# Optimization experiments

Measured on AMD Instinct MI355X. Metric: run time of the kernel, lower is better.

## Reference

```python
import jax, jax.numpy as jnp
import numpy as np

DIM = 1024
NH = 16
HD = DIM // NH  # 64
B, S = 4, 2048
EPS = 1e-5


def layer_norm(x, g, b):
    mu = jnp.mean(x, axis=-1, keepdims=True)
    var = jnp.mean(jnp.square(x - mu), axis=-1, keepdims=True)
    return (x - mu) * jax.lax.rsqrt(var + EPS) * g + b


def setup_inputs() -> dict:
    key = jax.random.key(0)
    ks = jax.random.split(key, 12)
    std = 0.02
    return {
        "x": jax.random.normal(ks[0], (B, S, DIM), jnp.float32),
        "ln1_g": jnp.ones((DIM,), jnp.float32),
        "ln1_b": jnp.zeros((DIM,), jnp.float32),
        # per-head Q/K/V linears stacked over heads: [NH, DIM, HD]
        "Wq": jax.random.normal(ks[1], (NH, DIM, HD), jnp.float32) * std,
        "bq": jnp.zeros((NH, HD), jnp.float32),
        "Wk": jax.random.normal(ks[2], (NH, DIM, HD), jnp.float32) * std,
        "bk": jnp.zeros((NH, HD), jnp.float32),
        "Wv": jax.random.normal(ks[3], (NH, DIM, HD), jnp.float32) * std,
        "bv": jnp.zeros((NH, HD), jnp.float32),
        "ln2_g": jnp.ones((DIM,), jnp.float32),
        "ln2_b": jnp.zeros((DIM,), jnp.float32),
        # FC block: LayerNorm -> Linear(dim,4dim) -> GELU -> Linear(4dim,dim) -> GELU
        "fcln_g": jnp.ones((DIM,), jnp.float32),
        "fcln_b": jnp.zeros((DIM,), jnp.float32),
        "W1": jax.random.normal(ks[4], (DIM, 4 * DIM), jnp.float32) * std,
        "b1": jnp.zeros((4 * DIM,), jnp.float32),
        "W2": jax.random.normal(ks[5], (4 * DIM, DIM), jnp.float32) * std,
        "b2": jnp.zeros((DIM,), jnp.float32),
    }


def reference(x, ln1_g, ln1_b, Wq, bq, Wk, bk, Wv, bv,
              ln2_g, ln2_b, fcln_g, fcln_b, W1, b1, W2, b2):
    # --- MHA branch: x + concat_h(head_h(ln1(x))) ---
    h = layer_norm(x, ln1_g, ln1_b)                       # [B,S,D]
    q = jnp.einsum('bsd,hdk->bhsk', h, Wq) + bq[None, :, None, :]
    k = jnp.einsum('bsd,hdk->bhsk', h, Wk) + bk[None, :, None, :]
    v = jnp.einsum('bsd,hdk->bhsk', h, Wv) + bv[None, :, None, :]
    scores = jnp.einsum('bhsk,bhtk->bhst', q, k) / jnp.sqrt(jnp.float32(HD))
    causal = jnp.tril(jnp.ones((S, S), bool))
    scores = jnp.where(causal[None, None], scores, jnp.float32(-1e9))
    attn = jax.nn.softmax(scores, axis=-1)                # [B,NH,S,S]
    o = jnp.einsum('bhst,bhtk->bhsk', attn, v)            # [B,NH,S,HD]
    o = o.transpose(0, 2, 1, 3).reshape(B, S, DIM)        # concat heads
    x = x + o
    # --- FC branch: x + GELU(GELU(LN(ln2(x)) @ W1) @ W2) ---
    h2 = layer_norm(x, ln2_g, ln2_b)
    h2 = layer_norm(h2, fcln_g, fcln_b)
    h2 = jax.nn.gelu(h2 @ W1 + b1, approximate=False)
    h2 = jax.nn.gelu(h2 @ W2 + b2, approximate=False)
    return x + h2
```

## Files before the change

kernel.cpp:

```cpp
#include <hip/hip_runtime.h>
#include <math.h>

#define DIMD 1024
#define NHD  16
#define HDD  64
#define BBB  4
#define SSS  2048
#define MMM  (BBB*SSS)

typedef __bf16 bf16;
typedef __bf16 bf16x8 __attribute__((ext_vector_type(8)));
typedef __bf16 bf16x4 __attribute__((ext_vector_type(4)));
typedef float  f32x4  __attribute__((ext_vector_type(4)));


__device__ __forceinline__ void gld16(const void* g, void* l) {
  __builtin_amdgcn_global_load_lds((const __attribute__((address_space(1))) void*)g,
                                   (__attribute__((address_space(3))) void*)l,
                                   16, 0, 0);
}

__device__ __forceinline__ f32x4 mfma_bf16(bf16x8 a, bf16x8 b, f32x4 c) {
  return __builtin_amdgcn_mfma_f32_16x16x32_bf16(a, b, c, 0, 0, 0);
}

__device__ __forceinline__ float gelu_f(float x) {
  const float u2 = 1.5957691216057308f * x * (1.0f + 0.044715f * x * x);
  const float e = __expf(u2);
  float r;
  asm("v_rcp_f32 %0, %1" : "=v"(r) : "v"(e + 1.0f));
  return x * (1.0f - r);
}

__device__ __forceinline__ void blockReduce2(float& s, float& s2, float* red) {
  #pragma unroll
  for (int m = 1; m < 64; m <<= 1) {
    s  += __shfl_xor(s,  m);
    s2 += __shfl_xor(s2, m);
  }
  const int wave = threadIdx.x >> 6, lane = threadIdx.x & 63;
  __syncthreads();
  if (lane == 0) { red[wave*2] = s; red[wave*2+1] = s2; }
  __syncthreads();
  s  = red[0] + red[2] + red[4] + red[6];
  s2 = red[1] + red[3] + red[5] + red[7];
}

#define SBAR() do { __builtin_amdgcn_sched_barrier(0); __builtin_amdgcn_s_barrier(); \
                    __builtin_amdgcn_sched_barrier(0); } while (0)
#define LGKM0() do { asm volatile("s_waitcnt lgkmcnt(0)" ::: "memory"); \
                     __builtin_amdgcn_sched_barrier(0); } while (0)
#define VMC(n)  do { asm volatile("s_waitcnt vmcnt(" #n ")" ::: "memory"); \
                     __builtin_amdgcn_sched_barrier(0); } while (0)


__global__ __launch_bounds__(256)
void transpose_k(const float* __restrict__ in, bf16* __restrict__ out, int R, int C) {
  __shared__ float tile[32][33];
  const int z = blockIdx.z;
  in  += (size_t)z * R * C;
  out += (size_t)z * R * C;
  const int r0 = blockIdx.x * 32, c0 = blockIdx.y * 32;
  const int tx = threadIdx.x, ty = threadIdx.y;
  #pragma unroll
  for (int k = 0; k < 4; ++k)
    tile[ty + k*8][tx] = in[(size_t)(r0 + ty + k*8) * C + c0 + tx];
  __syncthreads();
  #pragma unroll
  for (int k = 0; k < 4; ++k)
    out[(size_t)(c0 + ty + k*8) * R + r0 + tx] = (bf16)tile[tx][ty + k*8];
}


__global__ __launch_bounds__(256)
void transpose_qkv_k(const float* __restrict__ Wq, const float* __restrict__ Wk,
                     const float* __restrict__ Wv, bf16* __restrict__ out) {
  __shared__ float tile[32][33];
  const int z = blockIdx.z;
  const int which = z >> 4, zh = z & 15;
  const float* in = (which == 0 ? Wq : (which == 1 ? Wk : Wv)) + (size_t)zh * 1024 * 64;
  bf16* op = out + (size_t)z * 64 * 1024;
  const int r0 = blockIdx.x * 32, c0 = blockIdx.y * 32;
  const int tx = threadIdx.x, ty = threadIdx.y;
  #pragma unroll
  for (int k = 0; k < 4; ++k)
    tile[ty + k*8][tx] = in[(size_t)(r0 + ty + k*8) * 64 + c0 + tx];
  __syncthreads();
  #pragma unroll
  for (int k = 0; k < 4; ++k)
    op[(size_t)(c0 + ty + k*8) * 1024 + r0 + tx] = (bf16)tile[tx][ty + k*8];
}


__global__ __launch_bounds__(256)
void transpose_v_k(const bf16* __restrict__ in, bf16* __restrict__ out) {
  __shared__ bf16 t[64*72];
  const int z = blockIdx.y;
  const int s0 = blockIdx.x * 64;
  const bf16* ip = in + (size_t)z * SSS * HDD + (size_t)s0 * HDD;
  bf16* op = out + (size_t)z * SSS * HDD + s0;
  const int tid = threadIdx.x;
  #pragma unroll
  for (int p = 0; p < 2; ++p) {
    const int r = p*32 + (tid >> 3);
    const int c = (tid & 7) * 8;
    const int cs = c ^ (((r >> 3) & 7) << 3);
    *(bf16x8*)&t[r*72 + cs] = *(const bf16x8*)&ip[(size_t)r * HDD + c];
  }
  __syncthreads();
  #pragma unroll
  for (int p = 0; p < 2; ++p) {
    const int hd = p*32 + (tid >> 3);
    const int c0 = (tid & 7) * 8;
    bf16x8 v;
    #pragma unroll
    for (int j = 0; j < 8; ++j) {
      const int r = c0 + j;
      v[j] = t[r*72 + (hd ^ (((r >> 3) & 7) << 3))];
    }
    *(bf16x8*)&op[(size_t)hd * SSS + c0] = v;
  }
}


__global__ __launch_bounds__(256)
void ln1_k(const float* __restrict__ x, const float* __restrict__ g,
           const float* __restrict__ b, bf16* __restrict__ out) {
  __shared__ float red[8];
  const int row = blockIdx.x, t = threadIdx.x;
  const float4 v = ((const float4*)(x + (size_t)row * DIMD))[t];
  float s  = v.x + v.y + v.z + v.w;
  float s2 = v.x*v.x + v.y*v.y + v.z*v.z + v.w*v.w;
  blockReduce2(s, s2, red);
  const float mu   = s * (1.0f / DIMD);
  const float var  = s2 * (1.0f / DIMD) - mu * mu;
  const float rstd = rsqrtf(var + 1e-5f);
  const float4 gv = ((const float4*)g)[t];
  const float4 bv = ((const float4*)b)[t];
  bf16x4 o;
  o[0] = (bf16)((v.x - mu) * rstd * gv.x + bv.x);
  o[1] = (bf16)((v.y - mu) * rstd * gv.y + bv.y);
  o[2] = (bf16)((v.z - mu) * rstd * gv.z + bv.z);
  o[3] = (bf16)((v.w - mu) * rstd * gv.w + bv.w);
  *(bf16x4*)(out + (size_t)row * DIMD + t*4) = o;
}


__global__ __launch_bounds__(256)
void ln2fc_k(const float* __restrict__ x1,
             const float* __restrict__ g2, const float* __restrict__ b2,
             const float* __restrict__ g3, const float* __restrict__ b3,
             bf16* __restrict__ out) {
  __shared__ float red[8];
  const int row = blockIdx.x, t = threadIdx.x;
  const float4 v = ((const float4*)(x1 + (size_t)row * DIMD))[t];
  float s  = v.x + v.y + v.z + v.w;
  float s2 = v.x*v.x + v.y*v.y + v.z*v.z + v.w*v.w;
  blockReduce2(s, s2, red);
  float mu   = s * (1.0f / DIMD);
  float rstd = rsqrtf(s2 * (1.0f / DIMD) - mu * mu + 1e-5f);
  const float4 gv2 = ((const float4*)g2)[t];
  const float4 bv2 = ((const float4*)b2)[t];
  float y0 = (v.x - mu) * rstd * gv2.x + bv2.x;
  float y1 = (v.y - mu) * rstd * gv2.y + bv2.y;
  float y2 = (v.z - mu) * rstd * gv2.z + bv2.z;
  float y3 = (v.w - mu) * rstd * gv2.w + bv2.w;
  s  = y0 + y1 + y2 + y3;
  s2 = y0*y0 + y1*y1 + y2*y2 + y3*y3;
  blockReduce2(s, s2, red);
  mu   = s * (1.0f / DIMD);
  rstd = rsqrtf(s2 * (1.0f / DIMD) - mu * mu + 1e-5f);
  const float4 gv3 = ((const float4*)g3)[t];
  const float4 bv3 = ((const float4*)b3)[t];
  bf16x4 o;
  o[0] = (bf16)((y0 - mu) * rstd * gv3.x + bv3.x);
  o[1] = (bf16)((y1 - mu) * rstd * gv3.y + bv3.y);
  o[2] = (bf16)((y2 - mu) * rstd * gv3.z + bv3.z);
  o[3] = (bf16)((y3 - mu) * rstd * gv3.w + bv3.w);
  *(bf16x4*)(out + (size_t)row * DIMD + t*4) = o;
}


template<int MH2>
__device__ __forceinline__ void load_aH(bf16x8 (&d)[MH2][2], const bf16* base, int roff,
                                        int qv, int sw) {
  #pragma unroll
  for (int mi = 0; mi < MH2; ++mi)
    #pragma unroll
    for (int kk = 0; kk < 2; ++kk)
      d[mi][kk] = *(const bf16x8*)&base[roff + mi*1024 + (((kk<<2)+qv)^sw)*8];
}

__device__ __forceinline__ void load_b2(bf16x8 (&d)[2][2], const bf16* base, int roff,
                                        int qv, int sw) {
  #pragma unroll
  for (int nj = 0; nj < 2; ++nj)
    #pragma unroll
    for (int kk = 0; kk < 2; ++kk)
      d[nj][kk] = *(const bf16x8*)&base[roff + nj*1024 + (((kk<<2)+qv)^sw)*8];
}

template<int EPI, int MH2>
__global__ __launch_bounds__(512)
void gemm8p(const bf16* __restrict__ A, const bf16* __restrict__ Bt,
            int K, int N, int nbx,
            const float* __restrict__ bias, bf16* __restrict__ outB,
            float* __restrict__ outF,
            const float* __restrict__ bq, const float* __restrict__ bk,
            const float* __restrict__ bv) {
  constexpr int BM = 64 * MH2;
  __shared__ bf16 sA[2][BM*64];
  __shared__ bf16 sB[2][256*64];
  const int tid = threadIdx.x, wave = tid >> 6, lane = tid & 63;
  const int wm = wave >> 2, wn = wave & 3;

  const int q8 = gridDim.x >> 3;
  const int wg = (blockIdx.x & 7) * q8 + (blockIdx.x >> 3);
  const int by = wg / nbx, bx = wg - by * nbx;
  const int row0 = by * BM, col0 = bx * 256;

  const int l8 = lane >> 3, l7 = lane & 7;
  const int gsw = (l7 ^ l8) * 8;
  const int lo = lane & 15, qv = lane >> 4, sw = lane & 7;

  const bf16* Ags = A  + (size_t)(row0 + wave*8 + l8) * K + gsw;
  const bf16* Bgs = Bt + (size_t)(col0 + wave*8 + l8) * K + gsw;

  #define STAGE_A(buf, r, kt) gld16(Ags + (size_t)(r)*64*K + (kt), &sA[buf][(r)*4096 + wave*512])
  #define STAGE_B(buf, r, kt) gld16(Bgs + (size_t)(r)*64*K + (kt), &sB[buf][(r)*4096 + wave*512])

  const int fA = (wm*(32*MH2) + lo) * 64;
  const int fB = (wn*64       + lo) * 64;

  f32x4 acc[2*MH2][4] = {};
  bf16x8 a[MH2][2], b0[2][2], b1[2][2];
  const int NT = K >> 6;

  #pragma unroll
  for (int r = 0; r < MH2; ++r) STAGE_A(0, r, 0);
  #pragma unroll
  for (int r = 0; r < 4; ++r)   STAGE_B(0, r, 0);
  #pragma unroll
  for (int j = 0; j < MH2/2; ++j) STAGE_A(1, 2*j, 64);
  if (MH2 == 4) { VMC(2); } else { VMC(1); }
  SBAR();

  for (int t = 0; t < NT; ++t) {
    const int cur = t & 1, nxt = cur ^ 1;
    const int kt1 = (t + 1) << 6, kt2 = (t + 2) << 6;
    const bf16* cA = &sA[0][0] + cur * (BM*64);
    const bf16* cB = &sB[0][0] + cur * (256*64);

    load_aH<MH2>(a, cA, fA, qv, sw);
    load_b2(b0, cB, fB, qv, sw);
    if (t + 1 < NT) {
      #pragma unroll
      for (int j = 0; j < MH2/2; ++j) STAGE_A(nxt, 2*j + 1, kt1);
    }
    SBAR(); LGKM0();
    __builtin_amdgcn_s_setprio(1);
    #pragma unroll
    for (int mi = 0; mi < MH2; ++mi)
      #pragma unroll
      for (int nj = 0; nj < 2; ++nj)
        #pragma unroll
        for (int kk = 0; kk < 2; ++kk)
          acc[mi][nj] = mfma_bf16(a[mi][kk], b0[nj][kk], acc[mi][nj]);
    __builtin_amdgcn_s_setprio(0);
    SBAR();

    load_b2(b1, cB, fB + 2048, qv, sw);
    if (t + 1 < NT) { STAGE_B(nxt, 0, kt1); STAGE_B(nxt, 1, kt1); }
    SBAR(); LGKM0();
    __builtin_amdgcn_s_setprio(1);
    #pragma unroll
    for (int mi = 0; mi < MH2; ++mi)
      #pragma unroll
      for (int nj = 0; nj < 2; ++nj)
        #pragma unroll
        for (int kk = 0; kk < 2; ++kk)
          acc[mi][2+nj] = mfma_bf16(a[mi][kk], b1[nj][kk], acc[mi][2+nj]);
    __builtin_amdgcn_s_setprio(0);
    SBAR();

    load_aH<MH2>(a, cA, fA + MH2*1024, qv, sw);
    if (t + 1 < NT) { STAGE_B(nxt, 2, kt1); STAGE_B(nxt, 3, kt1); }
    SBAR(); LGKM0();
    __builtin_amdgcn_s_setprio(1);
    #pragma unroll
    for (int mi = 0; mi < MH2; ++mi)
      #pragma unroll
      for (int nj = 0; nj < 2; ++nj)
        #pragma unroll
        for (int kk = 0; kk < 2; ++kk)
          acc[MH2+mi][nj] = mfma_bf16(a[mi][kk], b0[nj][kk], acc[MH2+mi][nj]);
    __builtin_amdgcn_s_setprio(0);
    SBAR();

    if (t + 2 < NT) {
      #pragma unroll
      for (int j = 0; j < MH2/2; ++j) STAGE_A(cur, 2*j, kt2);
    }
    SBAR();
    __builtin_amdgcn_s_setprio(1);
    #pragma unroll
    for (int mi = 0; mi < MH2; ++mi)
      #pragma unroll
      for (int nj = 0; nj < 2; ++nj)
        #pragma unroll
        for (int kk = 0; kk < 2; ++kk)
          acc[MH2+mi][2+nj] = mfma_bf16(a[mi][kk], b1[nj][kk], acc[MH2+mi][2+nj]);
    __builtin_amdgcn_s_setprio(0);

    if (t + 1 < NT) {
      if (t + 2 < NT) { if (MH2 == 4) { VMC(2); } else { VMC(1); } }
      else            { VMC(0); }
      SBAR();
    }
  }
  #undef STAGE_A
  #undef STAGE_B

  #pragma unroll
  for (int mi = 0; mi < 2*MH2; ++mi)
    #pragma unroll
    for (int ni = 0; ni < 4; ++ni)
      #pragma unroll
      for (int i = 0; i < 4; ++i) {
        const int row = row0 + wm*(32*MH2) + mi*16 + qv*4 + i;
        const int col = col0 + wn*64 + ni*16 + lo;
        float v = acc[mi][ni][i];
        if (EPI == 0) {
          const int which = col >> 10, h = (col >> 6) & 15, hd = col & 63;
          const float* bp = (which == 0) ? bq : ((which == 1) ? bk : bv);
          v += bp[h*64 + hd];
          if (which == 0) v *= 0.125f;
          const int b_ = row >> 11, s_ = row & 2047;
          const size_t dst = ((((size_t)which*BBB + b_)*NHD + h)*SSS + s_)*HDD + hd;
          outB[dst] = (bf16)v;
        } else if (EPI == 1) {
          v = gelu_f(v + bias[col]);
          outB[(size_t)row * N + col] = (bf16)v;
        } else {
          v = gelu_f(v + bias[col]);
          outF[(size_t)row * N + col] += v;
        }
      }
}


__global__ __launch_bounds__(256)
void attn_k(const bf16* __restrict__ qkv, const bf16* __restrict__ Vt,
            const float* __restrict__ x, float* __restrict__ out) {
  __shared__ bf16 sK[64*72];
  __shared__ bf16 sVt[80*72];
  __shared__ bf16 sP[128*72];
  const int bh = blockIdx.y;
  const int b = bh >> 4, h = bh & 15;
  const int tid = threadIdx.x, wave = tid >> 6, lane = tid & 63;
  const size_t plane = (size_t)BBB * NHD * SSS * HDD;
  const bf16* Qp  = qkv + ((size_t)b * NHD + h) * SSS * HDD;
  const bf16* Kp  = Qp + plane;
  const bf16* Vtp = Vt + ((size_t)b * NHD + h) * SSS * HDD;

  const int r8 = tid >> 3;
  const int c8 = (tid & 7) * 8;

  for (int j = tid; j < 16*72; j += 256) sVt[64*72 + j] = (bf16)1.0f;

  for (int pass = 0; pass < 2; ++pass) {
    const int q0 = (pass == 0 ? (int)blockIdx.x : 15 - (int)blockIdx.x) * 128;

    bf16x8 aq[2][2];
    #pragma unroll
    for (int mi = 0; mi < 2; ++mi)
      #pragma unroll
      for (int kk = 0; kk < 2; ++kk)
        aq[mi][kk] = *(const bf16x8*)&Qp[(size_t)(q0 + wave*32 + mi*16 + (lane & 15)) * HDD
                                         + kk*32 + (lane >> 4) * 8];

    f32x4 o[2][5] = {};

    bf16x8 rk0, rk1, rv0, rv1;
    rk0 = *(const bf16x8*)&Kp[(size_t)r8 * HDD + c8];
    rk1 = *(const bf16x8*)&Kp[(size_t)(32 + r8) * HDD + c8];
    rv0 = *(const bf16x8*)&Vtp[(size_t)r8 * SSS + c8];
    rv1 = *(const bf16x8*)&Vtp[(size_t)(32 + r8) * SSS + c8];

    const int nt = (q0 + 128) / 64;
    for (int t = 0; t < nt; ++t) {
      const int kv0 = t * 64;
      __syncthreads();
      *(bf16x8*)&sK[r8*72 + c8]        = rk0;
      *(bf16x8*)&sK[(32 + r8)*72 + c8] = rk1;
      *(bf16x8*)&sVt[r8*72 + c8]        = rv0;
      *(bf16x8*)&sVt[(32 + r8)*72 + c8] = rv1;
      __syncthreads();
      if (t + 1 < nt) {
        const int kn = kv0 + 64;
        rk0 = *(const bf16x8*)&Kp[(size_t)(kn + r8) * HDD + c8];
        rk1 = *(const bf16x8*)&Kp[(size_t)(kn + 32 + r8) * HDD + c8];
        rv0 = *(const bf16x8*)&Vtp[(size_t)r8 * SSS + kn + c8];
        rv1 = *(const bf16x8*)&Vtp[(size_t)(32 + r8) * SSS + kn + c8];
      }
      if (kv0 <= q0 + wave*32 + 31) {
        f32x4 s[2][4] = {};
        #pragma unroll
        for (int kk = 0; kk < 2; ++kk)
          #pragma unroll
          for (int ni = 0; ni < 4; ++ni) {
            const bf16x8 bk_ = *(const bf16x8*)&sK[(ni*16 + (lane & 15))*72 + kk*32 + (lane >> 4)*8];
            s[0][ni] = mfma_bf16(aq[0][kk], bk_, s[0][ni]);
            s[1][ni] = mfma_bf16(aq[1][kk], bk_, s[1][ni]);
          }
        if (kv0 + 63 > q0 + wave*32) {
          #pragma unroll
          for (int mi = 0; mi < 2; ++mi)
            #pragma unroll
            for (int ni = 0; ni < 4; ++ni)
              #pragma unroll
              for (int i = 0; i < 4; ++i) {
                const int rg = q0 + wave*32 + mi*16 + (lane >> 4)*4 + i;
                const int cg = kv0 + ni*16 + (lane & 15);
                if (cg > rg) s[mi][ni][i] = -1e30f;
              }
        }
        #pragma unroll
        for (int mi = 0; mi < 2; ++mi)
          #pragma unroll
          for (int ni = 0; ni < 4; ++ni)
            #pragma unroll
            for (int i = 0; i < 4; ++i)
              sP[(wave*32 + mi*16 + (lane >> 4)*4 + i)*72 + ni*16 + (lane & 15)] =
                  (bf16)__expf(s[mi][ni][i]);
        asm volatile("s_waitcnt lgkmcnt(0)" ::: "memory");
        __builtin_amdgcn_sched_barrier(0);
        #pragma unroll
        for (int ks = 0; ks < 2; ++ks) {
          bf16x8 ap[2];
          ap[0] = *(const bf16x8*)&sP[(wave*32 +      (lane & 15))*72 + ks*32 + (lane >> 4)*8];
          ap[1] = *(const bf16x8*)&sP[(wave*32 + 16 + (lane & 15))*72 + ks*32 + (lane >> 4)*8];
          #pragma unroll
          for (int hf = 0; hf < 5; ++hf) {
            const bf16x8 bv_ = *(const bf16x8*)&sVt[(hf*16 + (lane & 15))*72 + ks*32 + (lane >> 4)*8];
            o[0][hf] = mfma_bf16(ap[0], bv_, o[0][hf]);
            o[1][hf] = mfma_bf16(ap[1], bv_, o[1][hf]);
          }
        }
      }
    }
    #pragma unroll
    for (int mi = 0; mi < 2; ++mi) {
      float inv[4];
      #pragma unroll
      for (int i = 0; i < 4; ++i) inv[i] = 1.0f / o[mi][4][i];
      #pragma unroll
      for (int hf = 0; hf < 4; ++hf)
        #pragma unroll
        for (int i = 0; i < 4; ++i) {
          const int srow = q0 + wave*32 + mi*16 + (lane >> 4)*4 + i;
          const int col  = h*HDD + hf*16 + (lane & 15);
          const size_t idx = ((size_t)b * SSS + srow) * DIMD + col;
          out[idx] = x[idx] + o[mi][hf][i] * inv[i];
        }
    }
  }
}


extern "C" void kernel_launch(void* const* d_in, const int* in_sizes, int n_in,
                              void* d_out, int out_size, void* d_ws, size_t ws_size,
                              hipStream_t stream) {
  const float* x     = (const float*)d_in[0];
  const float* ln1g  = (const float*)d_in[1];
  const float* ln1b  = (const float*)d_in[2];
  const float* Wq    = (const float*)d_in[3];
  const float* bq    = (const float*)d_in[4];
  const float* Wk    = (const float*)d_in[5];
  const float* bk    = (const float*)d_in[6];
  const float* Wv    = (const float*)d_in[7];
  const float* bv    = (const float*)d_in[8];
  const float* ln2g  = (const float*)d_in[9];
  const float* ln2b  = (const float*)d_in[10];
  const float* fclng = (const float*)d_in[11];
  const float* fclnb = (const float*)d_in[12];
  const float* W1    = (const float*)d_in[13];
  const float* b1    = (const float*)d_in[14];
  const float* W2    = (const float*)d_in[15];
  const float* b2    = (const float*)d_in[16];
  float* out = (float*)d_out;

  char* ws = (char*)d_ws;
  bf16* h     = (bf16*)(ws);
  bf16* Wqkvt = (bf16*)(ws + 16777216);
  bf16* W1t   = (bf16*)(ws + 23068672);
  bf16* W2t   = (bf16*)(ws + 31457280);
  bf16* qkv   = (bf16*)(ws + 39845888);
  bf16* u     = (bf16*)(ws + 39845888);
  bf16* VtB   = h;
  const size_t plane = (size_t)BBB * NHD * SSS * HDD;

  const dim3 tb(32, 8);
  transpose_qkv_k<<<dim3(32, 2, 48), tb, 0, stream>>>(Wq, Wk, Wv, Wqkvt);
  transpose_k<<<dim3(32, 128, 1), tb, 0, stream>>>(W1, W1t, 1024, 4096);
  transpose_k<<<dim3(128, 32, 1), tb, 0, stream>>>(W2, W2t, 4096, 1024);

  ln1_k<<<MMM, 256, 0, stream>>>(x, ln1g, ln1b, h);

  gemm8p<0,2><<<dim3(768), 512, 0, stream>>>(h, Wqkvt, 1024, 3072, 12,
                                             nullptr, qkv, nullptr, bq, bk, bv);

  transpose_v_k<<<dim3(SSS/64, BBB*NHD), 256, 0, stream>>>(qkv + 2*plane, VtB);

  attn_k<<<dim3(8, BBB*NHD), 256, 0, stream>>>(qkv, VtB, x, out);

  ln2fc_k<<<MMM, 256, 0, stream>>>(out, ln2g, ln2b, fclng, fclnb, h);

  gemm8p<1,4><<<dim3(512), 512, 0, stream>>>(h, W1t, 1024, 4096, 16,
                                             b1, u, nullptr, nullptr, nullptr, nullptr);

  gemm8p<2,2><<<dim3(256), 512, 0, stream>>>(u, W2t, 4096, 1024, 4,
                                             b2, nullptr, out, nullptr, nullptr, nullptr);
}
```

Measured before the change: 369.6 us.

## Load all LDS fragments upfront and use partial lgkmcnt waits in GEMM loop

Restructures the GEMM main loop so the A and B fragments for both halves are read from LDS at the start of each k-step into separate register sets. Partial lgkmcnt waits then let MFMAs start on the first fragments while later LDS reads are still in flight. All next-tile B staging is issued together, and several block barriers are dropped. This cuts barrier and wait stalls but raises register pressure, and it is delicate because the lgkmcnt counts must match how many LDS instructions each fragment load emits.

New measurement: 345.6 us. -6.5%, faster.

```diff
diff --git a/kernel.cpp b/kernel.cpp
--- a/kernel.cpp
+++ b/kernel.cpp
@@ -50,6 +50,8 @@
                     __builtin_amdgcn_sched_barrier(0); } while (0)
 #define LGKM0() do { asm volatile("s_waitcnt lgkmcnt(0)" ::: "memory"); \
                      __builtin_amdgcn_sched_barrier(0); } while (0)
+#define LGKMC(n) do { asm volatile("s_waitcnt lgkmcnt(" #n ")" ::: "memory"); \
+                      __builtin_amdgcn_sched_barrier(0); } while (0)
 #define VMC(n)  do { asm volatile("s_waitcnt vmcnt(" #n ")" ::: "memory"); \
                      __builtin_amdgcn_sched_barrier(0); } while (0)
 
@@ -233,7 +235,7 @@
   const int fB = (wn*64       + lo) * 64;
 
   f32x4 acc[2*MH2][4] = {};
-  bf16x8 a[MH2][2], b0[2][2], b1[2][2];
+  bf16x8 aL[MH2][2], aU[MH2][2], b0[2][2], b1[2][2];
   const int NT = K >> 6;
 
   #pragma unroll
@@ -251,13 +253,18 @@
     const bf16* cA = &sA[0][0] + cur * (BM*64);
     const bf16* cB = &sB[0][0] + cur * (256*64);
 
-    load_aH<MH2>(a, cA, fA, qv, sw);
+    load_aH<MH2>(aL, cA, fA, qv, sw);
     load_b2(b0, cB, fB, qv, sw);
+    load_b2(b1, cB, fB + 2048, qv, sw);
+    load_aH<MH2>(aU, cA, fA + MH2*1024, qv, sw);
     if (t + 1 < NT) {
       #pragma unroll
       for (int j = 0; j < MH2/2; ++j) STAGE_A(nxt, 2*j + 1, kt1);
+      #pragma unroll
+      for (int r = 0; r < 4; ++r)     STAGE_B(nxt, r, kt1);
     }
-    SBAR(); LGKM0();
+
+    if (MH2 == 4) { LGKMC(12); } else { LGKMC(8); }
     __builtin_amdgcn_s_setprio(1);
     #pragma unroll
     for (int mi = 0; mi < MH2; ++mi)
@@ -265,43 +272,27 @@
       for (int nj = 0; nj < 2; ++nj)
         #pragma unroll
         for (int kk = 0; kk < 2; ++kk)
-          acc[mi][nj] = mfma_bf16(a[mi][kk], b0[nj][kk], acc[mi][nj]);
+          acc[mi][nj] = mfma_bf16(aL[mi][kk], b0[nj][kk], acc[mi][nj]);
     __builtin_amdgcn_s_setprio(0);
+
+    if (MH2 == 4) { LGKMC(8); } else { LGKMC(4); }
+    __builtin_amdgcn_s_setprio(1);
+    #pragma unroll
+    for (int mi = 0; mi < MH2; ++mi)
+      #pragma unroll
+      for (int nj = 0; nj < 2; ++nj)
+        #pragma unroll
+        for (int kk = 0; kk < 2; ++kk)
+          acc[mi][2+nj] = mfma_bf16(aL[mi][kk], b1[nj][kk], acc[mi][2+nj]);
+    __builtin_amdgcn_s_setprio(0);
+
+    LGKM0();
     SBAR();
-
-    load_b2(b1, cB, fB + 2048, qv, sw);
-    if (t + 1 < NT) { STAGE_B(nxt, 0, kt1); STAGE_B(nxt, 1, kt1); }
-    SBAR(); LGKM0();
-    __builtin_amdgcn_s_setprio(1);
-    #pragma unroll
-    for (int mi = 0; mi < MH2; ++mi)
-      #pragma unroll
-      for (int nj = 0; nj < 2; ++nj)
-        #pragma unroll
-        for (int kk = 0; kk < 2; ++kk)
-          acc[mi][2+nj] = mfma_bf16(a[mi][kk], b1[nj][kk], acc[mi][2+nj]);
-    __builtin_amdgcn_s_setprio(0);
-    SBAR();
-
-    load_aH<MH2>(a, cA, fA + MH2*1024, qv, sw);
-    if (t + 1 < NT) { STAGE_B(nxt, 2, kt1); STAGE_B(nxt, 3, kt1); }
-    SBAR(); LGKM0();
-    __builtin_amdgcn_s_setprio(1);
-    #pragma unroll
-    for (int mi = 0; mi < MH2; ++mi)
-      #pragma unroll
-      for (int nj = 0; nj < 2; ++nj)
-        #pragma unroll
-        for (int kk = 0; kk < 2; ++kk)
-          acc[MH2+mi][nj] = mfma_bf16(a[mi][kk], b0[nj][kk], acc[MH2+mi][nj]);
-    __builtin_amdgcn_s_setprio(0);
-    SBAR();
-
     if (t + 2 < NT) {
       #pragma unroll
       for (int j = 0; j < MH2/2; ++j) STAGE_A(cur, 2*j, kt2);
     }
-    SBAR();
+
     __builtin_amdgcn_s_setprio(1);
     #pragma unroll
     for (int mi = 0; mi < MH2; ++mi)
@@ -309,7 +300,14 @@
       for (int nj = 0; nj < 2; ++nj)
         #pragma unroll
         for (int kk = 0; kk < 2; ++kk)
-          acc[MH2+mi][2+nj] = mfma_bf16(a[mi][kk], b1[nj][kk], acc[MH2+mi][2+nj]);
+          acc[MH2+mi][nj] = mfma_bf16(aU[mi][kk], b0[nj][kk], acc[MH2+mi][nj]);
+    #pragma unroll
+    for (int mi = 0; mi < MH2; ++mi)
+      #pragma unroll
+      for (int nj = 0; nj < 2; ++nj)
+        #pragma unroll
+        for (int kk = 0; kk < 2; ++kk)
+          acc[MH2+mi][2+nj] = mfma_bf16(aU[mi][kk], b1[nj][kk], acc[MH2+mi][2+nj]);
     __builtin_amdgcn_s_setprio(0);
 
     if (t + 1 < NT) {
```
